# Kernel optimization log

Measured on AMD Instinct MI355X. Metric: run time of the kernel, lower is better.

The kernel has to match this reference:

```python
import jax, jax.numpy as jnp
import numpy as np

DIM = 1024
NUM_HEAD = 16
DIM_HEAD = DIM // NUM_HEAD
RMS_EPS = 1.1920929e-07  # torch.finfo(float32).eps (nn.RMSNorm default eps=None)
EPS_LIN = 1e-6
THETA = 10000.0


def rmsnorm(x, g, eps=RMS_EPS):
    return x * jax.lax.rsqrt(jnp.mean(x * x, axis=-1, keepdims=True) + eps) * g


def rope_cos_sin(seq_len, dim_head, dtype=jnp.float32):
    inv_freq = 1.0 / (THETA ** (jnp.arange(0, dim_head, 2, dtype=dtype) / dim_head))
    t = jnp.arange(seq_len, dtype=dtype)
    freqs = jnp.outer(t, inv_freq)  # [L, dh//2]
    return jnp.cos(freqs), jnp.sin(freqs)


def apply_rope(t, cos, sin):
    # t: [b, h, L, dh]; pairs are (t[...,2i], t[...,2i+1]) viewed as complex
    tr = t[..., 0::2]
    ti = t[..., 1::2]
    out_r = tr * cos - ti * sin
    out_i = tr * sin + ti * cos
    return jnp.stack([out_r, out_i], axis=-1).reshape(t.shape)


def setup_inputs() -> dict:
    key = jax.random.key(0)
    ks = jax.random.split(key, 5)
    B, L = 4, 4096
    x = jax.random.normal(ks[0], (B, L, DIM), dtype=jnp.float32)
    Wqkv = jax.random.normal(ks[1], (3 * DIM, DIM), dtype=jnp.float32) * 0.02
    bqkv = jax.random.normal(ks[2], (3 * DIM,), dtype=jnp.float32) * 0.02
    gq = jnp.ones((DIM,), dtype=jnp.float32)
    gk = jnp.ones((DIM,), dtype=jnp.float32)
    Wout = jax.random.normal(ks[3], (DIM, DIM), dtype=jnp.float32) * 0.02
    bout = jax.random.normal(ks[4], (DIM,), dtype=jnp.float32) * 0.02
    gout = jnp.ones((DIM,), dtype=jnp.float32)
    return {"x": x, "Wqkv": Wqkv, "bqkv": bqkv, "gq": gq, "gk": gk,
            "Wout": Wout, "bout": bout, "gout": gout}


def reference(x, Wqkv, bqkv, gq, gk, Wout, bout, gout):
    B, L, D = x.shape
    qkv = x @ Wqkv.T + bqkv  # [B, L, 3D]
    q, k, v = jnp.split(qkv, 3, axis=-1)
    q = rmsnorm(q, gq)
    k = rmsnorm(k, gk)
    # b L (h d) -> b h L d
    split = lambda t: t.reshape(B, L, NUM_HEAD, DIM_HEAD).transpose(0, 2, 1, 3)
    q, k, v = split(q), split(k), split(v)
    cos, sin = rope_cos_sin(L, DIM_HEAD)  # start_pos = 0 (default)
    cos = cos[None, None]  # [1,1,L,dh//2]
    sin = sin[None, None]
    q = apply_rope(q, cos, sin)
    k = apply_rope(k, cos, sin)
    # linear attention: ReLU feature map + padded-value normalization trick
    qf = jax.nn.relu(q)
    kf = jax.nn.relu(k)
    vpad = jnp.concatenate([v, jnp.ones_like(v[..., :1])], axis=-1)  # pad_val=1.0
    vk = jnp.einsum('bhlp,bhld->bhpd', vpad, kf)       # [b,h,dh+1,dh]
    res = jnp.einsum('bhpd,bhld->bhlp', vk, qf)        # [b,h,L,dh+1]
    attn = res[..., :-1] / (res[..., -1:] + EPS_LIN)
    attn = attn.transpose(0, 2, 1, 3).reshape(B, L, D)  # b h L d -> b L (h d)
    out = rmsnorm(attn @ Wout.T + bout, gout)
    return out
```

## Files before the change

kernel.cpp:

```cpp
#include <hip/hip_runtime.h>
#include <stdint.h>

#define RMS_EPS 1.1920929e-07f
#define EPS_LIN 1e-6f

typedef __attribute__((ext_vector_type(8))) short bf16x8;
typedef __attribute__((ext_vector_type(4))) float f32x4;

__device__ __forceinline__ unsigned short f2bf(float f) {
  union { float f; unsigned int u; } v; v.f = f;
  unsigned int r = v.u + 0x7fffu + ((v.u >> 16) & 1u);
  return (unsigned short)(r >> 16);
}
__device__ __forceinline__ float bf2f(unsigned short s) {
  union { unsigned int u; float f; } v; v.u = ((unsigned int)s) << 16;
  return v.f;
}

__global__ __launch_bounds__(256) void k_init(
    const float* __restrict__ x, const float* __restrict__ Wqkv,
    const float* __restrict__ Wout,
    unsigned short* __restrict__ xb, unsigned short* __restrict__ wqkvb,
    unsigned short* __restrict__ woutb,
    float* __restrict__ cosT, float* __restrict__ sinT) {
  const int blk = blockIdx.x;
  const int t = threadIdx.x;
  if (blk < 20480) {
    const float* src;
    unsigned short* dst;
    int base;
    if (blk < 16384) { src = x; dst = xb; base = blk; }
    else if (blk < 19456) { src = Wqkv; dst = wqkvb; base = blk - 16384; }
    else { src = Wout; dst = woutb; base = blk - 19456; }
    int i = (base * 256 + t) * 4;
    float4 v = *reinterpret_cast<const float4*>(src + i);
    ushort4 o = { f2bf(v.x), f2bf(v.y), f2bf(v.z), f2bf(v.w) };
    *reinterpret_cast<ushort4*>(dst + i) = o;
  } else {
    int idx = (blk - 20480) * 256 + t;
    int l = idx >> 5, i = idx & 31;
    float inv_freq = expf(-((float)(2 * i) / 64.0f) * logf(10000.0f));
    float ang = (float)l * inv_freq;
    cosT[idx] = cosf(ang);
    sinT[idx] = sinf(ang);
  }
}

__device__ __forceinline__ void stage16(const unsigned short* g, unsigned short* lds_base,
                                        int lane) {
#if __has_builtin(__builtin_amdgcn_global_load_lds)
  __builtin_amdgcn_global_load_lds(
      (const __attribute__((address_space(1))) unsigned int*)g,
      (__attribute__((address_space(3))) unsigned int*)lds_base, 16, 0, 0);
#else
  *reinterpret_cast<uint4*>(lds_base + lane * 8) = *reinterpret_cast<const uint4*>(g);
#endif
}

__global__ __launch_bounds__(256, 3) void k_gemm_bt(
    const unsigned short* __restrict__ A, const unsigned short* __restrict__ Bw,
    const float* __restrict__ bias, int M, int N, int K, int mode,
    unsigned short* __restrict__ qb, unsigned short* __restrict__ kb,
    unsigned short* __restrict__ vb, unsigned short* __restrict__ preb) {
  __shared__ unsigned short As[128 * 64];
  __shared__ unsigned short Bs[128 * 64];
  const int nt = N >> 7;
  const int bm = blockIdx.x / nt, bn = blockIdx.x % nt;
  const int m0 = bm << 7, n0 = bn << 7;
  const int t = threadIdx.x;
  const int wave = t >> 6, lane = t & 63;
  const int wr = wave >> 1, wc = wave & 1;
  const int quad = lane >> 4, m16 = lane & 15;

  const unsigned short* ApS[4];
  const unsigned short* BpS[4];
  unsigned short* AlS[4];
  unsigned short* BlS[4];
#pragma unroll
  for (int s = 0; s < 4; ++s) {
    int u = wave * 256 + s * 64 + lane;
    int row = u >> 3;
    int ku = (u & 7) ^ (row & 7);
    ApS[s] = A + (size_t)(m0 + row) * K + ku * 8;
    BpS[s] = Bw + (size_t)(n0 + row) * K + ku * 8;
    AlS[s] = As + (size_t)(wave * 256 + s * 64) * 8;
    BlS[s] = Bs + (size_t)(wave * 256 + s * 64) * 8;
  }

  int offA[4][2], offB[4][2];
#pragma unroll
  for (int i = 0; i < 4; ++i) {
    int rowA = wr * 64 + i * 16 + m16;
    int rowB = wc * 64 + i * 16 + m16;
#pragma unroll
    for (int ks = 0; ks < 2; ++ks) {
      int kuf = ks * 4 + quad;
      offA[i][ks] = (rowA * 8 + (kuf ^ (rowA & 7))) * 8;
      offB[i][ks] = (rowB * 8 + (kuf ^ (rowB & 7))) * 8;
    }
  }

  f32x4 acc[4][4] = {};

  for (int k0 = 0; k0 < K; k0 += 64) {
#pragma unroll
    for (int s = 0; s < 4; ++s) {
      stage16(ApS[s] + k0, AlS[s], lane);
      stage16(BpS[s] + k0, BlS[s], lane);
    }
    __syncthreads();
#pragma unroll
    for (int ks = 0; ks < 2; ++ks) {
      bf16x8 fa[4], fb[4];
#pragma unroll
      for (int i = 0; i < 4; ++i)
        fa[i] = *reinterpret_cast<const bf16x8*>(As + offA[i][ks]);
#pragma unroll
      for (int j = 0; j < 4; ++j)
        fb[j] = *reinterpret_cast<const bf16x8*>(Bs + offB[j][ks]);
#pragma unroll
      for (int i = 0; i < 4; ++i)
#pragma unroll
        for (int j = 0; j < 4; ++j)
          acc[i][j] = __builtin_amdgcn_mfma_f32_16x16x32_bf16(fa[i], fb[j], acc[i][j], 0, 0, 0);
    }
    __syncthreads();
  }

#pragma unroll
  for (int i = 0; i < 4; ++i) {
    int rbase = m0 + wr * 64 + i * 16 + quad * 4;
#pragma unroll
    for (int j = 0; j < 4; ++j) {
      int col = n0 + wc * 64 + j * 16 + m16;
      float bc = bias[col];
#pragma unroll
      for (int r = 0; r < 4; ++r) {
        int row = rbase + r;
        float val = acc[i][j][r] + bc;
        unsigned short bv = f2bf(val);
        if (mode == 0) {
          if (col < 1024) {
            qb[(size_t)row * 1024 + col] = bv;
          } else if (col < 2048) {
            kb[(size_t)row * 1024 + (col - 1024)] = bv;
          } else {
            int h = (col - 2048) >> 6, d = col & 63;
            int b = row >> 12, l = row & 4095;
            vb[(((size_t)(b * 16 + h)) * 4096 + l) * 64 + d] = bv;
          }
        } else {
          preb[(size_t)row * N + col] = bv;
        }
      }
    }
  }
}

__global__ __launch_bounds__(256) void k_qknorm(
    const unsigned short* __restrict__ qb, const unsigned short* __restrict__ kb,
    const float* __restrict__ gq, const float* __restrict__ gk,
    const float* __restrict__ cosT, const float* __restrict__ sinT,
    unsigned short* __restrict__ qfb, unsigned short* __restrict__ kfb) {
  const int wid = (blockIdx.x << 2) + (threadIdx.x >> 6);
  const int row = wid >> 1;
  const int which = wid & 1;
  const int lane = threadIdx.x & 63;
  const int l = row & 4095;
  const int b = row >> 12;
  const unsigned short* src = (which ? kb : qb) + (size_t)row * 1024 + lane * 16;
  const float* g = which ? gk : gq;
  unsigned short* dstb = which ? kfb : qfb;

  bf16x8 u0 = *reinterpret_cast<const bf16x8*>(src);
  bf16x8 u1 = *reinterpret_cast<const bf16x8*>(src + 8);
  float v[16];
  float ss = 0.f;
#pragma unroll
  for (int e = 0; e < 8; ++e) {
    v[e] = bf2f((unsigned short)u0[e]);
    v[8 + e] = bf2f((unsigned short)u1[e]);
  }
#pragma unroll
  for (int e = 0; e < 16; ++e) ss += v[e] * v[e];
#pragma unroll
  for (int off = 1; off < 64; off <<= 1) ss += __shfl_xor(ss, off, 64);
  const float sc = rsqrtf(ss * (1.0f / 1024.0f) + RMS_EPS);

  const float* gp = g + lane * 16;
  const float* cp = cosT + l * 32 + (lane & 3) * 8;
  const float* sp = sinT + l * 32 + (lane & 3) * 8;
  bf16x8 o0, o1;
#pragma unroll
  for (int p = 0; p < 8; ++p) {
    float cc = cp[p], sv = sp[p];
    float x0 = v[2 * p] * sc * gp[2 * p];
    float x1 = v[2 * p + 1] * sc * gp[2 * p + 1];
    float r0 = x0 * cc - x1 * sv;
    float r1 = x0 * sv + x1 * cc;
    unsigned short b0 = f2bf(fmaxf(r0, 0.f));
    unsigned short b1 = f2bf(fmaxf(r1, 0.f));
    if (p < 4) { o0[2 * p] = (short)b0; o0[2 * p + 1] = (short)b1; }
    else { o1[2 * (p - 4)] = (short)b0; o1[2 * (p - 4) + 1] = (short)b1; }
  }
  unsigned short* dp =
      dstb + (((size_t)(b * 16 + (lane >> 2))) * 4096 + l) * 64 + (lane & 3) * 16;
  *reinterpret_cast<bf16x8*>(dp) = o0;
  *reinterpret_cast<bf16x8*>(dp + 8) = o1;
}

__global__ __launch_bounds__(256) void k_vk(const unsigned short* __restrict__ vb,
                                            const unsigned short* __restrict__ kfb,
                                            float* __restrict__ part) {
  const int bh = blockIdx.x >> 4;
  const int chunk = blockIdx.x & 15;
  const int t = threadIdx.x;
  const int wv = t >> 6, lane = t & 63;
  const int quad = lane >> 4, m16 = lane & 15;

  __shared__ __align__(16) unsigned short Vt[64 * 40];
  __shared__ __align__(16) unsigned short Kt[64 * 40];
  __shared__ float dred[4][64];

  f32x4 acc[4] = {};
  float accD = 0.f;

  for (int tile = 0; tile < 8; ++tile) {
    const size_t rbase =
        ((size_t)bh * 4096 + chunk * 256 + tile * 32 + wv * 8) * 64 + lane;
    bf16x8 vv, kv;
#pragma unroll
    for (int j = 0; j < 8; ++j) {
      unsigned short ve = vb[rbase + j * 64];
      unsigned short ke = kfb[rbase + j * 64];
      vv[j] = (short)ve;
      kv[j] = (short)ke;
      accD += bf2f(ke);
    }
    *reinterpret_cast<bf16x8*>(Vt + lane * 40 + wv * 8) = vv;
    *reinterpret_cast<bf16x8*>(Kt + lane * 40 + wv * 8) = kv;
    __syncthreads();

    bf16x8 fa = *reinterpret_cast<const bf16x8*>(Vt + (wv * 16 + m16) * 40 + quad * 8);
#pragma unroll
    for (int j = 0; j < 4; ++j) {
      bf16x8 fb = *reinterpret_cast<const bf16x8*>(Kt + (j * 16 + m16) * 40 + quad * 8);
      acc[j] = __builtin_amdgcn_mfma_f32_16x16x32_bf16(fa, fb, acc[j], 0, 0, 0);
    }
    __syncthreads();
  }

  float* dst = part + ((size_t)chunk * 64 + bh) * 4160;
#pragma unroll
  for (int j = 0; j < 4; ++j)
#pragma unroll
    for (int r = 0; r < 4; ++r)
      dst[(wv * 16 + quad * 4 + r) * 64 + j * 16 + m16] = acc[j][r];

  dred[wv][lane] = accD;
  __syncthreads();
  if (t < 64) dst[64 * 64 + t] = dred[0][t] + dred[1][t] + dred[2][t] + dred[3][t];
}

__global__ __launch_bounds__(256) void k_vkred(const float* __restrict__ part,
                                               float* __restrict__ vk) {
  const int i = (blockIdx.x * 256 + threadIdx.x) * 4;
  float4 s = *reinterpret_cast<const float4*>(part + i);
#pragma unroll
  for (int c = 1; c < 16; ++c) {
    float4 r = *reinterpret_cast<const float4*>(part + (size_t)c * 266240 + i);
    s.x += r.x; s.y += r.y; s.z += r.z; s.w += r.w;
  }
  *reinterpret_cast<float4*>(vk + i) = s;
}

__global__ __launch_bounds__(256) void k_res(const unsigned short* __restrict__ qfb,
                                             const float* __restrict__ vk,
                                             unsigned short* __restrict__ attnb) {
  const int bh = blockIdx.x >> 5;
  const int lt = (blockIdx.x & 31) << 7;
  const int b = bh >> 4, h = bh & 15;
  const int t = threadIdx.x;
  const int wave = t >> 6, lane = t & 63;
  __shared__ unsigned short Aq[128 * 64];
  __shared__ unsigned short Bv[64 * 64];
  __shared__ float vkD[64];
  __shared__ float invden[128];

  const unsigned short* Ag = qfb + ((size_t)bh * 4096 + lt) * 64;
#pragma unroll
  for (int s = 0; s < 4; ++s)
    stage16(Ag + wave * 2048 + s * 512 + lane * 8, Aq + wave * 2048 + s * 512, lane);

  const float* vsrc = vk + (size_t)bh * 65 * 64;
  {
    int base = t * 16;
#pragma unroll
    for (int c = 0; c < 4; ++c) {
      float4 f = *reinterpret_cast<const float4*>(vsrc + base + c * 4);
      ushort4 o = { f2bf(f.x), f2bf(f.y), f2bf(f.z), f2bf(f.w) };
      *reinterpret_cast<ushort4*>(Bv + base + c * 4) = o;
    }
  }
  if (t < 64) vkD[t] = vsrc[64 * 64 + t];
  __syncthreads();

  f32x4 acc[2][4] = {};
  const int quad = lane >> 4, m16 = lane & 15;
#pragma unroll
  for (int step = 0; step < 2; ++step) {
    bf16x8 fa[2], fb[4];
#pragma unroll
    for (int i = 0; i < 2; ++i)
      fa[i] = *reinterpret_cast<const bf16x8*>(Aq + (wave * 32 + i * 16 + m16) * 64 +
                                               step * 32 + quad * 8);
#pragma unroll
    for (int j = 0; j < 4; ++j)
      fb[j] = *reinterpret_cast<const bf16x8*>(Bv + (j * 16 + m16) * 64 +
                                               step * 32 + quad * 8);
#pragma unroll
    for (int i = 0; i < 2; ++i)
#pragma unroll
      for (int j = 0; j < 4; ++j)
        acc[i][j] = __builtin_amdgcn_mfma_f32_16x16x32_bf16(fa[i], fb[j], acc[i][j], 0, 0, 0);
  }

  {
    const unsigned short* qr = Aq + (t >> 1) * 64 + (t & 1) * 32;
    const float* vd = vkD + (t & 1) * 32;
    float ds = 0.f;
#pragma unroll
    for (int c = 0; c < 4; ++c) {
      bf16x8 qv = *reinterpret_cast<const bf16x8*>(qr + c * 8);
#pragma unroll
      for (int j = 0; j < 8; ++j)
        ds += bf2f((unsigned short)qv[j]) * vd[c * 8 + j];
    }
    ds += __shfl_xor(ds, 1, 64);
    if ((t & 1) == 0) invden[t >> 1] = 1.0f / (ds + EPS_LIN);
  }
  __syncthreads();

#pragma unroll
  for (int i = 0; i < 2; ++i) {
#pragma unroll
    for (int r = 0; r < 4; ++r) {
      int row = wave * 32 + i * 16 + quad * 4 + r;
      float inv = invden[row];
      unsigned short* dst = attnb + ((size_t)(b * 4096 + lt + row)) * 1024 + h * 64;
#pragma unroll
      for (int j = 0; j < 4; ++j)
        dst[j * 16 + m16] = f2bf(acc[i][j][r] * inv);
    }
  }
}

__global__ __launch_bounds__(256) void k_outnorm(const unsigned short* __restrict__ preb,
                                                 const float* __restrict__ gout,
                                                 float* __restrict__ out) {
  const int row = (blockIdx.x << 2) + (threadIdx.x >> 6);
  const int lane = threadIdx.x & 63;
  const unsigned short* src = preb + (size_t)row * 1024 + lane * 16;
  float* drow = out + (size_t)row * 1024 + lane * 16;
  bf16x8 a0 = *reinterpret_cast<const bf16x8*>(src);
  bf16x8 a1 = *reinterpret_cast<const bf16x8*>(src + 8);
  float v[16];
  float ss = 0.f;
#pragma unroll
  for (int e = 0; e < 8; ++e) {
    v[e] = bf2f((unsigned short)a0[e]);
    v[8 + e] = bf2f((unsigned short)a1[e]);
  }
#pragma unroll
  for (int e = 0; e < 16; ++e) ss += v[e] * v[e];
#pragma unroll
  for (int off = 1; off < 64; off <<= 1) ss += __shfl_xor(ss, off, 64);
  const float sc = rsqrtf(ss * (1.0f / 1024.0f) + RMS_EPS);
  const float* gp = gout + lane * 16;
#pragma unroll
  for (int c = 0; c < 4; ++c) {
    float4 o = { v[c * 4 + 0] * sc * gp[c * 4 + 0], v[c * 4 + 1] * sc * gp[c * 4 + 1],
                 v[c * 4 + 2] * sc * gp[c * 4 + 2], v[c * 4 + 3] * sc * gp[c * 4 + 3] };
    *reinterpret_cast<float4*>(drow + c * 4) = o;
  }
}

#define OFF_XB     0ull
#define OFF_WQKVB  33554432ull
#define OFF_WOUTB  39845888ull
#define OFF_QB     41943040ull
#define OFF_KB     75497472ull
#define OFF_VB     109051904ull
#define OFF_QFB    142606336ull
#define OFF_KFB    176160768ull
#define OFF_VK     209715200ull
#define OFF_ATTNB  210780160ull
#define OFF_COST   244334592ull
#define OFF_SINT   244858880ull
#define WS_NEEDED  245383168ull

extern "C" void kernel_launch(void* const* d_in, const int* in_sizes, int n_in,
                              void* d_out, int out_size, void* d_ws, size_t ws_size,
                              hipStream_t stream) {
  const float* x    = (const float*)d_in[0];
  const float* Wqkv = (const float*)d_in[1];
  const float* bqkv = (const float*)d_in[2];
  const float* gq   = (const float*)d_in[3];
  const float* gk   = (const float*)d_in[4];
  const float* Wout = (const float*)d_in[5];
  const float* bout = (const float*)d_in[6];
  const float* gout = (const float*)d_in[7];

  if (ws_size < WS_NEEDED) return;

  char* ws = (char*)d_ws;
  unsigned short* xb    = (unsigned short*)(ws + OFF_XB);
  unsigned short* wqkvb = (unsigned short*)(ws + OFF_WQKVB);
  unsigned short* woutb = (unsigned short*)(ws + OFF_WOUTB);
  unsigned short* qb    = (unsigned short*)(ws + OFF_QB);
  unsigned short* kb    = (unsigned short*)(ws + OFF_KB);
  unsigned short* vb    = (unsigned short*)(ws + OFF_VB);
  unsigned short* qfb   = (unsigned short*)(ws + OFF_QFB);
  unsigned short* kfb   = (unsigned short*)(ws + OFF_KFB);
  float*          vkbuf = (float*)(ws + OFF_VK);
  unsigned short* attnb = (unsigned short*)(ws + OFF_ATTNB);
  float*          cosT  = (float*)(ws + OFF_COST);
  float*          sinT  = (float*)(ws + OFF_SINT);
  unsigned short* preb  = (unsigned short*)(ws + OFF_QB);
  float*          vkpart = (float*)(ws + OFF_ATTNB);

  k_init<<<20992, 256, 0, stream>>>(x, Wqkv, Wout, xb, wqkvb, woutb, cosT, sinT);

  k_gemm_bt<<<128 * 24, 256, 0, stream>>>(xb, wqkvb, bqkv, 16384, 3072, 1024, 0,
                                          qb, kb, vb, nullptr);
  k_qknorm<<<8192, 256, 0, stream>>>(qb, kb, gq, gk, cosT, sinT, qfb, kfb);

  k_vk<<<1024, 256, 0, stream>>>(vb, kfb, vkpart);
  k_vkred<<<260, 256, 0, stream>>>(vkpart, vkbuf);

  k_res<<<2048, 256, 0, stream>>>(qfb, vkbuf, attnb);

  k_gemm_bt<<<128 * 8, 256, 0, stream>>>(attnb, woutb, bout, 16384, 1024, 1024, 1,
                                         nullptr, nullptr, nullptr, preb);
  k_outnorm<<<4096, 256, 0, stream>>>(preb, gout, (float*)d_out);
}
```

Measured before the change: 372.3 us.

## Fuse QK norm, RoPE and ReLU into consumers, keeping only row scales

The separate q/k normalization kernel that wrote normalized, rotated, ReLU'd q and k in head-major layout is replaced by a small kernel that only computes per-row RMS scales. The vk and res kernels now read raw q/k from the GEMM output and apply scale, gain, RoPE and ReLU on the fly. This removes the write and re-read of two full bf16 activation tensors. In exchange, k_vk does strided 2-byte loads with duplicated partner reads from the row-major layout, which may coalesce poorly.

```diff
diff --git a/kernel.cpp b/kernel.cpp
--- a/kernel.cpp
+++ b/kernel.cpp
@@ -157,85 +157,75 @@
   }
 }
 
-__global__ __launch_bounds__(256) void k_qknorm(
+__global__ __launch_bounds__(256) void k_scales(
     const unsigned short* __restrict__ qb, const unsigned short* __restrict__ kb,
-    const float* __restrict__ gq, const float* __restrict__ gk,
-    const float* __restrict__ cosT, const float* __restrict__ sinT,
-    unsigned short* __restrict__ qfb, unsigned short* __restrict__ kfb) {
+    float* __restrict__ scq, float* __restrict__ sck) {
   const int wid = (blockIdx.x << 2) + (threadIdx.x >> 6);
   const int row = wid >> 1;
   const int which = wid & 1;
   const int lane = threadIdx.x & 63;
-  const int l = row & 4095;
-  const int b = row >> 12;
   const unsigned short* src = (which ? kb : qb) + (size_t)row * 1024 + lane * 16;
-  const float* g = which ? gk : gq;
-  unsigned short* dstb = which ? kfb : qfb;
-
   bf16x8 u0 = *reinterpret_cast<const bf16x8*>(src);
   bf16x8 u1 = *reinterpret_cast<const bf16x8*>(src + 8);
-  float v[16];
   float ss = 0.f;
 #pragma unroll
   for (int e = 0; e < 8; ++e) {
-    v[e] = bf2f((unsigned short)u0[e]);
-    v[8 + e] = bf2f((unsigned short)u1[e]);
-  }
-#pragma unroll
-  for (int e = 0; e < 16; ++e) ss += v[e] * v[e];
+    float a = bf2f((unsigned short)u0[e]);
+    float b = bf2f((unsigned short)u1[e]);
+    ss += a * a + b * b;
+  }
 #pragma unroll
   for (int off = 1; off < 64; off <<= 1) ss += __shfl_xor(ss, off, 64);
-  const float sc = rsqrtf(ss * (1.0f / 1024.0f) + RMS_EPS);
-
-  const float* gp = g + lane * 16;
-  const float* cp = cosT + l * 32 + (lane & 3) * 8;
-  const float* sp = sinT + l * 32 + (lane & 3) * 8;
-  bf16x8 o0, o1;
-#pragma unroll
-  for (int p = 0; p < 8; ++p) {
-    float cc = cp[p], sv = sp[p];
-    float x0 = v[2 * p] * sc * gp[2 * p];
-    float x1 = v[2 * p + 1] * sc * gp[2 * p + 1];
-    float r0 = x0 * cc - x1 * sv;
-    float r1 = x0 * sv + x1 * cc;
-    unsigned short b0 = f2bf(fmaxf(r0, 0.f));
-    unsigned short b1 = f2bf(fmaxf(r1, 0.f));
-    if (p < 4) { o0[2 * p] = (short)b0; o0[2 * p + 1] = (short)b1; }
-    else { o1[2 * (p - 4)] = (short)b0; o1[2 * (p - 4) + 1] = (short)b1; }
-  }
-  unsigned short* dp =
-      dstb + (((size_t)(b * 16 + (lane >> 2))) * 4096 + l) * 64 + (lane & 3) * 16;
-  *reinterpret_cast<bf16x8*>(dp) = o0;
-  *reinterpret_cast<bf16x8*>(dp + 8) = o1;
+  if (lane == 0) (which ? sck : scq)[row] = rsqrtf(ss * (1.0f / 1024.0f) + RMS_EPS);
 }
 
 __global__ __launch_bounds__(256) void k_vk(const unsigned short* __restrict__ vb,
-                                            const unsigned short* __restrict__ kfb,
+                                            const unsigned short* __restrict__ kb,
+                                            const float* __restrict__ gk,
+                                            const float* __restrict__ cosT,
+                                            const float* __restrict__ sinT,
+                                            const float* __restrict__ sck,
                                             float* __restrict__ part) {
   const int bh = blockIdx.x >> 4;
   const int chunk = blockIdx.x & 15;
+  const int b = bh >> 4, h = bh & 15;
   const int t = threadIdx.x;
   const int wv = t >> 6, lane = t & 63;
   const int quad = lane >> 4, m16 = lane & 15;
+  const int d = lane;
 
   __shared__ __align__(16) unsigned short Vt[64 * 40];
   __shared__ __align__(16) unsigned short Kt[64 * 40];
   __shared__ float dred[4][64];
 
+  const float gs = gk[h * 64 + d];
+  const float gp = gk[h * 64 + (d ^ 1)];
+  const int odd = d & 1;
+
   f32x4 acc[4] = {};
   float accD = 0.f;
 
   for (int tile = 0; tile < 8; ++tile) {
-    const size_t rbase =
-        ((size_t)bh * 4096 + chunk * 256 + tile * 32 + wv * 8) * 64 + lane;
+    const int l0 = chunk * 256 + tile * 32 + wv * 8;
     bf16x8 vv, kv;
 #pragma unroll
     for (int j = 0; j < 8; ++j) {
-      unsigned short ve = vb[rbase + j * 64];
-      unsigned short ke = kfb[rbase + j * 64];
+      const int l = l0 + j;
+      const size_t vrow = ((size_t)bh * 4096 + l) * 64;
+      const size_t krow = ((size_t)(b * 4096 + l)) * 1024 + h * 64;
+      unsigned short ve = vb[vrow + d];
+      unsigned short kraw = kb[krow + d];
+      unsigned short kpar = kb[krow + (d ^ 1)];
+      const float scr = sck[b * 4096 + l];
+      float xs = bf2f(kraw) * scr * gs;
+      float xp = bf2f(kpar) * scr * gp;
+      float cc = cosT[l * 32 + (d >> 1)];
+      float sn = sinT[l * 32 + (d >> 1)];
+      float r = odd ? (xp * sn + xs * cc) : (xs * cc - xp * sn);
+      unsigned short kf = f2bf(fmaxf(r, 0.f));
       vv[j] = (short)ve;
-      kv[j] = (short)ke;
-      accD += bf2f(ke);
+      kv[j] = (short)kf;
+      accD += bf2f(kf);
     }
     *reinterpret_cast<bf16x8*>(Vt + lane * 40 + wv * 8) = vv;
     *reinterpret_cast<bf16x8*>(Kt + lane * 40 + wv * 8) = kv;
@@ -274,7 +264,11 @@
   *reinterpret_cast<float4*>(vk + i) = s;
 }
 
-__global__ __launch_bounds__(256) void k_res(const unsigned short* __restrict__ qfb,
+__global__ __launch_bounds__(256) void k_res(const unsigned short* __restrict__ qb,
+                                             const float* __restrict__ gq,
+                                             const float* __restrict__ cosT,
+                                             const float* __restrict__ sinT,
+                                             const float* __restrict__ scq,
                                              const float* __restrict__ vk,
                                              unsigned short* __restrict__ attnb) {
   const int bh = blockIdx.x >> 5;
@@ -287,10 +281,35 @@
   __shared__ float vkD[64];
   __shared__ float invden[128];
 
-  const unsigned short* Ag = qfb + ((size_t)bh * 4096 + lt) * 64;
-#pragma unroll
-  for (int s = 0; s < 4; ++s)
-    stage16(Ag + wave * 2048 + s * 512 + lane * 8, Aq + wave * 2048 + s * 512, lane);
+  {
+    const int rl = lane >> 3;
+    const int dd = (lane & 7) * 8;
+    const float4 g0 = *reinterpret_cast<const float4*>(gq + h * 64 + dd);
+    const float4 g1 = *reinterpret_cast<const float4*>(gq + h * 64 + dd + 4);
+    const float gg[8] = { g0.x, g0.y, g0.z, g0.w, g1.x, g1.y, g1.z, g1.w };
+#pragma unroll
+    for (int s = 0; s < 4; ++s) {
+      const int r_loc = wave * 32 + s * 8 + rl;
+      const int l = lt + r_loc;
+      const int row = b * 4096 + l;
+      bf16x8 u = *reinterpret_cast<const bf16x8*>(qb + (size_t)row * 1024 + h * 64 + dd);
+      const float scr = scq[row];
+      const float* cp = cosT + l * 32 + (dd >> 1);
+      const float* sp = sinT + l * 32 + (dd >> 1);
+      bf16x8 o;
+#pragma unroll
+      for (int p = 0; p < 4; ++p) {
+        float x0 = bf2f((unsigned short)u[2 * p]) * scr * gg[2 * p];
+        float x1 = bf2f((unsigned short)u[2 * p + 1]) * scr * gg[2 * p + 1];
+        float cc = cp[p], sn = sp[p];
+        float r0 = x0 * cc - x1 * sn;
+        float r1 = x0 * sn + x1 * cc;
+        o[2 * p] = (short)f2bf(fmaxf(r0, 0.f));
+        o[2 * p + 1] = (short)f2bf(fmaxf(r1, 0.f));
+      }
+      *reinterpret_cast<bf16x8*>(Aq + wave * 2048 + s * 512 + lane * 8) = o;
+    }
+  }
 
   const float* vsrc = vk + (size_t)bh * 65 * 64;
   {
@@ -420,8 +439,8 @@
   unsigned short* qb    = (unsigned short*)(ws + OFF_QB);
   unsigned short* kb    = (unsigned short*)(ws + OFF_KB);
   unsigned short* vb    = (unsigned short*)(ws + OFF_VB);
-  unsigned short* qfb   = (unsigned short*)(ws + OFF_QFB);
-  unsigned short* kfb   = (unsigned short*)(ws + OFF_KFB);
+  float*          scq   = (float*)(ws + OFF_QFB);
+  float*          sck   = (float*)(ws + OFF_QFB + 65536ull);
   float*          vkbuf = (float*)(ws + OFF_VK);
   unsigned short* attnb = (unsigned short*)(ws + OFF_ATTNB);
   float*          cosT  = (float*)(ws + OFF_COST);
@@ -433,12 +452,13 @@
 
   k_gemm_bt<<<128 * 24, 256, 0, stream>>>(xb, wqkvb, bqkv, 16384, 3072, 1024, 0,
                                           qb, kb, vb, nullptr);
-  k_qknorm<<<8192, 256, 0, stream>>>(qb, kb, gq, gk, cosT, sinT, qfb, kfb);
-
-  k_vk<<<1024, 256, 0, stream>>>(vb, kfb, vkpart);
+
+  k_scales<<<8192, 256, 0, stream>>>(qb, kb, scq, sck);
+
+  k_vk<<<1024, 256, 0, stream>>>(vb, kb, gk, cosT, sinT, sck, vkpart);
   k_vkred<<<260, 256, 0, stream>>>(vkpart, vkbuf);
 
-  k_res<<<2048, 256, 0, stream>>>(qfb, vkbuf, attnb);
+  k_res<<<2048, 256, 0, stream>>>(qb, gq, cosT, sinT, scq, vkbuf, attnb);
 
   k_gemm_bt<<<128 * 8, 256, 0, stream>>>(attnb, woutb, bout, 16384, 1024, 1024, 1,
                                          nullptr, nullptr, nullptr, preb);
```

Result: no change. 374.0 us (+0.5%).
